# Optimization experiments

Hardware: AMD Instinct MI355X
Metric: run time of the kernel (lower is better)

Reference implementation:

```python
import jax, jax.numpy as jnp
import numpy as np

B, KL, XL, DIM, H, PB = 4, 128, 4096, 256, 8, 8
HD = DIM // H
SCALE = HD ** -0.5
N_DIS = 64 + 2


def setup_inputs() -> dict:
    key = jax.random.key(0)
    ks = jax.random.split(key, 10)
    x = jax.random.normal(ks[0], (B, XL, DIM), jnp.float32)
    kernal = jax.random.normal(ks[1], (B, KL, DIM), jnp.float32)
    rd = jax.random.randint(ks[2], (B, KL, XL), 0, N_DIS)
    polar_pos = jax.random.randint(ks[3], (B, KL, XL), 0, PB)
    att_mask = jax.random.uniform(ks[4], (B, H, XL, KL)) < 0.1
    W_qkv = jax.random.normal(ks[5], (DIM, 3 * DIM), jnp.float32) * 0.02
    dis_embed = jax.random.normal(ks[6], (N_DIS, H), jnp.float32) * 0.02
    polar_emb = jax.random.normal(ks[7], (PB, 1), jnp.float32) * 0.02
    W_proj = jax.random.normal(ks[8], (DIM, DIM), jnp.float32) * 0.02
    b_proj = jnp.zeros((DIM,), jnp.float32)
    return dict(x=x, kernal=kernal, rd=rd, polar_pos=polar_pos, att_mask=att_mask,
                W_qkv=W_qkv, dis_embed=dis_embed, polar_emb=polar_emb,
                W_proj=W_proj, b_proj=b_proj)


def _heads(t, h):
    b, n, d = t.shape
    return t.reshape(b, n, h, d // h).transpose(0, 2, 1, 3)  # b h n hd


def reference(x, kernal, rd, polar_pos, att_mask, W_qkv, dis_embed, polar_emb, W_proj, b_proj):
    b, xl, dim = x.shape
    kl = kernal.shape[1]
    h = H
    scale = (dim // h) ** -0.5

    q, k, v = [_heads(t, h) for t in jnp.split(x @ W_qkv, 3, axis=-1)]        # b h xl hd
    k_q, k_k, k_v = [_heads(t, h) for t in jnp.split(kernal @ W_qkv, 3, axis=-1)]  # b h kl hd

    rd_e = dis_embed[rd].transpose(0, 3, 1, 2)  # (b,kl,xl,h) -> (b,h,kl,xl)

    # kernel -> x attention scores
    k_x_attn = jnp.einsum('bhkd,bhxd->bhkx', k_q, k) * scale  # b h kl xl

    # main orientation: one-hot-weighted |attn| reduced over x, argmax over polar bins
    pp = jnp.broadcast_to(polar_pos[:, None], (b, h, kl, xl))  # b h kl xl
    polar_hot = jax.nn.one_hot(pp, PB, dtype=k_x_attn.dtype)   # b h kl xl o
    ori_sum = jnp.einsum('bhkx,bhkxo->bhko', jnp.abs(k_x_attn), polar_hot)
    main_ori = jnp.argmax(ori_sum, axis=-1)                    # b h kl
    new_polar = pp - main_ori[..., None]
    new_polar = jnp.where(new_polar < 0, new_polar + PB, new_polar)
    polar_bias = polar_emb[new_polar, 0]                       # b h kl xl

    mask_k = att_mask.transpose(0, 1, 3, 2)                    # b h kl xl
    k_x_attn = jnp.where(mask_k, jnp.asarray(-1e6, k_x_attn.dtype), k_x_attn)
    attn_k = jax.nn.softmax(k_x_attn + rd_e + polar_bias, axis=-1)
    k_out = jnp.einsum('bhkx,bhxd->bhkd', attn_k, v)
    k_out = k_out.transpose(0, 2, 1, 3).reshape(b, kl, dim) @ W_proj + b_proj

    # x -> kernel attention scores
    x_k_attn = jnp.einsum('bhxd,bhkd->bhxk', q, k_k) * scale   # b h xl kl
    x_k_attn = jnp.where(att_mask, jnp.asarray(-1e9, x_k_attn.dtype), x_k_attn)
    x_k_attn = jax.nn.softmax(x_k_attn + rd_e.transpose(0, 1, 3, 2)
                              + polar_bias.transpose(0, 1, 3, 2), axis=-1)
    x_out = jnp.einsum('bhxk,bhkd->bhxd', x_k_attn, k_v)
    x_out = x_out.transpose(0, 2, 1, 3).reshape(b, xl, dim) @ W_proj + b_proj

    return (x_out, k_out)
```

## Files before the change

kernel.cpp:

```cpp
#include <hip/hip_runtime.h>
#include <hip/hip_bf16.h>

#define B_    4
#define KL_   128
#define XL_   4096
#define DIM_  256
#define H_    8
#define HD_   32
#define PB_   8
#define NDIS_ 66
#define TDIM_ 768
#define SCALE_ 0.17677669529663687f
#define NS_   4
#define XCH_  (XL_ / NS_)
#define NCH2_ 64
#define KC2_  16

typedef float v4f __attribute__((ext_vector_type(4)));
typedef short v8s __attribute__((ext_vector_type(8)));

__device__ __forceinline__ unsigned short f2bf(float f) {
    __hip_bfloat16 h = __float2bfloat16(f);
    return __builtin_bit_cast(unsigned short, h);
}
__device__ __forceinline__ float bf2f(unsigned short u) {
    return __bfloat162float(__builtin_bit_cast(__hip_bfloat16, u));
}
__device__ __forceinline__ void cvt_hilo(float v, unsigned short& hi, unsigned short& lo) {
    hi = f2bf(v);
    lo = f2bf(v - bf2f(hi));
}

__global__ __launch_bounds__(256) void pack_mask(const int* __restrict__ att_mask,
                                                 unsigned int* __restrict__ mbits) {
    size_t wid = (size_t)blockIdx.x * 256 + threadIdx.x;
    const int* src = &att_mask[wid * 32];
    unsigned bits = 0;
#pragma unroll
    for (int i = 0; i < 8; ++i) {
        int4 m4 = *(const int4*)&src[i * 4];
        bits |= (m4.x ? 1u : 0u) << (i * 4 + 0);
        bits |= (m4.y ? 1u : 0u) << (i * 4 + 1);
        bits |= (m4.z ? 1u : 0u) << (i * 4 + 2);
        bits |= (m4.w ? 1u : 0u) << (i * 4 + 3);
    }
    mbits[wid] = bits;
}

__global__ __launch_bounds__(256) void cvt_mat(const float* __restrict__ A,
                                               unsigned short* __restrict__ Ah,
                                               unsigned short* __restrict__ Al,
                                               size_t n4) {
    size_t i = ((size_t)blockIdx.x * 256 + threadIdx.x);
    if (i >= n4) return;
    float4 v = *(const float4*)&A[i * 4];
    ushort4 h, l;
    cvt_hilo(v.x, h.x, l.x);
    cvt_hilo(v.y, h.y, l.y);
    cvt_hilo(v.z, h.z, l.z);
    cvt_hilo(v.w, h.w, l.w);
    *(ushort4*)&Ah[i * 4] = h;
    *(ushort4*)&Al[i * 4] = l;
}

__global__ __launch_bounds__(256) void cvt_wT(const float* __restrict__ W,
                                              unsigned short* __restrict__ Wh,
                                              unsigned short* __restrict__ Wl,
                                              int K, int N) {
    int n = blockIdx.x, k = threadIdx.x;
    float v = W[(size_t)k * N + n];
    unsigned short h, l;
    cvt_hilo(v, h, l);
    Wh[(size_t)n * K + k] = h;
    Wl[(size_t)n * K + k] = l;
}

__global__ __launch_bounds__(256) void cvt_kq(const float* __restrict__ qkv_k,
                                              unsigned short* __restrict__ Kqh_g,
                                              unsigned short* __restrict__ Kql_g) {
    const int bh = blockIdx.x;
    const int b = bh >> 3, h = bh & 7;
    const int tid = threadIdx.x;
    const int k = tid >> 1, dg = (tid & 1) * 16;
    const float* src = &qkv_k[((size_t)(b * KL_ + k)) * TDIM_ + h * HD_ + dg];
    unsigned short hi[16], lo[16];
#pragma unroll
    for (int j4 = 0; j4 < 4; ++j4) {
        float4 v = *(const float4*)&src[j4 * 4];
        cvt_hilo(v.x, hi[j4 * 4 + 0], lo[j4 * 4 + 0]);
        cvt_hilo(v.y, hi[j4 * 4 + 1], lo[j4 * 4 + 1]);
        cvt_hilo(v.z, hi[j4 * 4 + 2], lo[j4 * 4 + 2]);
        cvt_hilo(v.w, hi[j4 * 4 + 3], lo[j4 * 4 + 3]);
    }
    unsigned short* dh = &Kqh_g[((size_t)bh * KL_ + k) * HD_ + dg];
    unsigned short* dl = &Kql_g[((size_t)bh * KL_ + k) * HD_ + dg];
    *(uint4*)&dh[0] = *(uint4*)&hi[0];
    *(uint4*)&dh[8] = *(uint4*)&hi[8];
    *(uint4*)&dl[0] = *(uint4*)&lo[0];
    *(uint4*)&dl[8] = *(uint4*)&lo[8];
}

__global__ __launch_bounds__(256) void gemm_mfma(const unsigned short* __restrict__ Ah,
                                                 const unsigned short* __restrict__ Al,
                                                 const unsigned short* __restrict__ Bh,
                                                 const unsigned short* __restrict__ Bl,
                                                 float* __restrict__ C,
                                                 const float* __restrict__ bias,
                                                 int M, int N, int K) {
    __shared__ __align__(16) unsigned short Ah_s[128 * 32];
    __shared__ __align__(16) unsigned short Al_s[128 * 32];
    __shared__ __align__(16) unsigned short Bh_s[128 * 32];
    __shared__ __align__(16) unsigned short Bl_s[128 * 32];
    const int tid = threadIdx.x;
    const int w = tid >> 6, lane = tid & 63;
    const int c = lane & 15, q = lane >> 4;
    const int bm = blockIdx.y * 128, bn = blockIdx.x * 128;

    const int lrow = lane >> 2;
    const int lcol = (lane & 3) * 8;

    v4f acc[2][8] = {};
    for (int k0 = 0; k0 < K; k0 += 32) {
        __syncthreads();
#pragma unroll
        for (int i = 0; i < 2; ++i) {
            const int chunk = w * 2 + i;
            const int row = chunk * 16 + lrow;
            const size_t ga = (size_t)(bm + row) * K + k0 + lcol;
            const size_t gb = (size_t)(bn + row) * K + k0 + lcol;
            const int lo = chunk * 512;
            __builtin_amdgcn_global_load_lds(
                (const __attribute__((address_space(1))) unsigned int*)&Ah[ga],
                (__attribute__((address_space(3))) unsigned int*)&Ah_s[lo], 16, 0, 0);
            __builtin_amdgcn_global_load_lds(
                (const __attribute__((address_space(1))) unsigned int*)&Al[ga],
                (__attribute__((address_space(3))) unsigned int*)&Al_s[lo], 16, 0, 0);
            __builtin_amdgcn_global_load_lds(
                (const __attribute__((address_space(1))) unsigned int*)&Bh[gb],
                (__attribute__((address_space(3))) unsigned int*)&Bh_s[lo], 16, 0, 0);
            __builtin_amdgcn_global_load_lds(
                (const __attribute__((address_space(1))) unsigned int*)&Bl[gb],
                (__attribute__((address_space(3))) unsigned int*)&Bl_s[lo], 16, 0, 0);
        }
        asm volatile("s_waitcnt vmcnt(0)" ::: "memory");
        __syncthreads();
        v8s afh[2], afl[2];
#pragma unroll
        for (int mt = 0; mt < 2; ++mt) {
            afh[mt] = *(v8s*)&Ah_s[(w * 32 + mt * 16 + c) * 32 + q * 8];
            afl[mt] = *(v8s*)&Al_s[(w * 32 + mt * 16 + c) * 32 + q * 8];
        }
#pragma unroll
        for (int nt = 0; nt < 8; ++nt) {
            v8s bfh = *(v8s*)&Bh_s[(nt * 16 + c) * 32 + q * 8];
            v8s bfl = *(v8s*)&Bl_s[(nt * 16 + c) * 32 + q * 8];
#pragma unroll
            for (int mt = 0; mt < 2; ++mt) {
                acc[mt][nt] = __builtin_amdgcn_mfma_f32_16x16x32_bf16(afl[mt], bfh, acc[mt][nt], 0, 0, 0);
                acc[mt][nt] = __builtin_amdgcn_mfma_f32_16x16x32_bf16(afh[mt], bfl, acc[mt][nt], 0, 0, 0);
                acc[mt][nt] = __builtin_amdgcn_mfma_f32_16x16x32_bf16(afh[mt], bfh, acc[mt][nt], 0, 0, 0);
            }
        }
    }
#pragma unroll
    for (int mt = 0; mt < 2; ++mt) {
#pragma unroll
        for (int nt = 0; nt < 8; ++nt) {
            int col = bn + nt * 16 + c;
            float bv = bias ? bias[col] : 0.0f;
#pragma unroll
            for (int r = 0; r < 4; ++r) {
                int row = bm + w * 32 + mt * 16 + q * 4 + r;
                C[(size_t)row * N + col] = acc[mt][nt][r] + bv;
            }
        }
    }
}

__global__ __launch_bounds__(256) void gemm64(const float* __restrict__ A,
                                              const float* __restrict__ Bw,
                                              float* __restrict__ C,
                                              const float* __restrict__ bias,
                                              int M, int N, int K) {
    __shared__ __align__(16) float As[16][68];
    __shared__ __align__(16) float Bs[16][64];
    const int tid = threadIdx.x;
    const int tx = tid & 15, ty = tid >> 4;
    const int bn = blockIdx.x * 64, bm = blockIdx.y * 64;
    const int am = tid >> 2, ac = tid & 3;
    float acc[4][4] = {};
    for (int k0 = 0; k0 < K; k0 += 16) {
        float4 a4 = *(const float4*)&A[(size_t)(bm + am) * K + k0 + ac * 4];
        As[ac * 4 + 0][am] = a4.x;
        As[ac * 4 + 1][am] = a4.y;
        As[ac * 4 + 2][am] = a4.z;
        As[ac * 4 + 3][am] = a4.w;
        *(float4*)&Bs[ty][tx * 4] = *(const float4*)&Bw[(size_t)(k0 + ty) * N + bn + tx * 4];
        __syncthreads();
#pragma unroll
        for (int kk = 0; kk < 16; ++kk) {
            float4 av = *(const float4*)&As[kk][ty * 4];
            float4 bv = *(const float4*)&Bs[kk][tx * 4];
            float a[4] = {av.x, av.y, av.z, av.w};
            float b[4] = {bv.x, bv.y, bv.z, bv.w};
#pragma unroll
            for (int i = 0; i < 4; ++i)
#pragma unroll
                for (int j = 0; j < 4; ++j) acc[i][j] += a[i] * b[j];
        }
        __syncthreads();
    }
#pragma unroll
    for (int i = 0; i < 4; ++i) {
        int m = bm + ty * 4 + i;
#pragma unroll
        for (int j = 0; j < 4; ++j) {
            int n = bn + tx * 4 + j;
            float v = acc[i][j];
            if (bias) v += bias[n];
            C[(size_t)m * N + n] = v;
        }
    }
}

__global__ __launch_bounds__(256) void score_bins_mfma4(const float* __restrict__ qkv_x,
                                                        const unsigned short* __restrict__ Kqh_g,
                                                        const unsigned short* __restrict__ Kql_g,
                                                        const int* __restrict__ rd,
                                                        const int* __restrict__ polar_pos,
                                                        const unsigned int* __restrict__ mbits,
                                                        const float* __restrict__ dis_embed,
                                                        __hip_bfloat16* __restrict__ Sg,
                                                        float* __restrict__ binspart) {
    const int b = blockIdx.z, h = blockIdx.y, xc = blockIdx.x;
    const int x0 = xc * 64;
    const int tid = threadIdx.x;
    const int w = tid >> 6, lane = tid & 63;
    const int c15 = lane & 15, q = lane >> 4;
    const size_t bh = (size_t)(b * H_ + h);

    __shared__ unsigned int mskb[64][5];
    __shared__ float de_h[NDIS_];
    __shared__ float binsL[8][4][16][PB_];

    {
        int xr = tid >> 2, kg = tid & 3;
        mskb[xr][kg] = mbits[(bh * XL_ + x0 + xr) * 4 + kg];
    }
    if (tid < NDIS_) de_h[tid] = dis_embed[tid * H_ + h];
    __syncthreads();

    v8s axh, axl;
    {
        const float* src = &qkv_x[((size_t)b * XL_ + x0 + w * 16 + c15) * TDIM_ + DIM_ + h * HD_ + q * 8];
        float4 v0 = *(const float4*)&src[0];
        float4 v1 = *(const float4*)&src[4];
        float vv[8] = {v0.x, v0.y, v0.z, v0.w, v1.x, v1.y, v1.z, v1.w};
#pragma unroll
        for (int j = 0; j < 8; ++j) {
            unsigned short hi, lo;
            cvt_hilo(vv[j], hi, lo);
            ((short*)&axh)[j] = (short)hi;
            ((short*)&axl)[j] = (short)lo;
        }
    }

    v8s bqh[2], bql[2];
    int4 r4[2], p4[2];
    auto load_nt = [&](int nt, int s) {
        const int k = nt * 16 + c15;
        const size_t kqoff = (bh * KL_ + k) * HD_ + q * 8;
        bqh[s] = *(const v8s*)&Kqh_g[kqoff];
        bql[s] = *(const v8s*)&Kql_g[kqoff];
        const size_t rowoff = ((size_t)(b * KL_ + k)) * XL_ + x0 + w * 16 + q * 4;
        r4[s] = *(const int4*)&rd[rowoff];
        p4[s] = *(const int4*)&polar_pos[rowoff];
    };
    load_nt(0, 0);

#pragma unroll
    for (int nt = 0; nt < 8; ++nt) {
        const int s = nt & 1;
        if (nt < 7) load_nt(nt + 1, s ^ 1);

        const int k = nt * 16 + c15;
        v4f D = {0.f, 0.f, 0.f, 0.f};
        D = __builtin_amdgcn_mfma_f32_16x16x32_bf16(axl, bqh[s], D, 0, 0, 0);
        D = __builtin_amdgcn_mfma_f32_16x16x32_bf16(axh, bql[s], D, 0, 0, 0);
        D = __builtin_amdgcn_mfma_f32_16x16x32_bf16(axh, bqh[s], D, 0, 0, 0);

        float bins[PB_] = {};
        {
            int rv[4] = {r4[s].x, r4[s].y, r4[s].z, r4[s].w};
            int pv[4] = {p4[s].x, p4[s].y, p4[s].z, p4[s].w};
            ushort4 pack;
#pragma unroll
            for (int r = 0; r < 4; ++r) {
                float sc = D[r] * SCALE_;
                float a = fabsf(sc);
                int pp = pv[r];
#pragma unroll
                for (int pb = 0; pb < PB_; ++pb) bins[pb] += (pp == pb) ? a : 0.0f;
                int xloc = w * 16 + q * 4 + r;
                int mbit = (mskb[xloc][k >> 5] >> (k & 31)) & 1;
                float sp = (mbit ? -1e6f : sc) + de_h[rv[r]];
                ((unsigned short*)&pack)[r] = f2bf(sp);
            }
            *(ushort4*)((unsigned short*)Sg + (bh * KL_ + k) * XL_ + x0 + w * 16 + q * 4) = pack;
        }

#pragma unroll
        for (int pb = 0; pb < PB_; ++pb) {
            bins[pb] += __shfl_xor(bins[pb], 16);
            bins[pb] += __shfl_xor(bins[pb], 32);
        }
        if (q == 0) {
#pragma unroll
            for (int pb = 0; pb < PB_; ++pb) binsL[nt][w][c15][pb] = bins[pb];
        }
    }
    __syncthreads();
    {
        int k = tid >> 1, half = tid & 1;
        int nt = k >> 4, c = k & 15;
        float4 s = {0.f, 0.f, 0.f, 0.f};
#pragma unroll
        for (int w4 = 0; w4 < 4; ++w4) {
            float4 v = *(float4*)&binsL[nt][w4][c][half * 4];
            s.x += v.x; s.y += v.y; s.z += v.z; s.w += v.w;
        }
        *(float4*)&binspart[(bh * KL_ + k) * (NCH2_ * PB_) + xc * PB_ + half * 4] = s;
    }
}

__global__ __launch_bounds__(256) void bins_argmax(const float* __restrict__ binspart,
                                                   int* __restrict__ main_ori) {
    const int w = threadIdx.x >> 6, lane = threadIdx.x & 63;
    const int row = blockIdx.x * 4 + w;
    float s[PB_];
#pragma unroll
    for (int pb = 0; pb < PB_; ++pb) s[pb] = 0.0f;
    if (lane < NCH2_) {
        const float* bp = &binspart[(size_t)row * (NCH2_ * PB_) + lane * PB_];
#pragma unroll
        for (int pb = 0; pb < PB_; ++pb) s[pb] = bp[pb];
    }
#pragma unroll
    for (int m = 1; m < 64; m <<= 1)
#pragma unroll
        for (int pb = 0; pb < PB_; ++pb) s[pb] += __shfl_xor(s[pb], m);
    if (lane == 0) {
        float best = s[0];
        int bi = 0;
#pragma unroll
        for (int pb = 1; pb < PB_; ++pb)
            if (s[pb] > best) { best = s[pb]; bi = pb; }
        main_ori[row] = bi;
    }
}

__global__ __launch_bounds__(256) void flash_cached2(const float* __restrict__ qkv_x,
                                                     const __hip_bfloat16* __restrict__ Sg,
                                                     const int* __restrict__ polar_pos,
                                                     const float* __restrict__ polar_emb,
                                                     const int* __restrict__ main_ori,
                                                     float* __restrict__ part) {
    const int b = blockIdx.z, h = blockIdx.y;
    const int kch = blockIdx.x / NS_, xc = blockIdx.x % NS_;
    const int k0 = kch * KC2_;
    const int tid = threadIdx.x;
    const int ki = tid >> 4, xt = tid & 15;

    __shared__ __align__(16) float4 vs[64][9];
    __shared__ int pol_s[KC2_][68];
    __shared__ float pe[PB_];

    if (tid < PB_) pe[tid] = polar_emb[tid];
    const size_t xbase = (size_t)b * XL_;
    const size_t bh = (size_t)(b * H_ + h);
    const size_t row_k = bh * KL_ + k0 + ki;
    const int mo = main_ori[row_k];
    const int xbeg = xc * XCH_;

    float l = 0.f;
    float4 acc[8] = {};
    __syncthreads();
    for (int t = 0; t < XCH_ / 64; ++t) {
        const int x0 = xbeg + t * 64;
        __syncthreads();
#pragma unroll
        for (int i = 0; i < 2; ++i) {
            int id = tid + 256 * i;
            int row = id >> 3, c = id & 7;
            vs[row][c] = *(const float4*)&qkv_x[(xbase + x0 + row) * TDIM_ + 2 * DIM_ + h * HD_ + c * 4];
        }
        {
            int kk = tid >> 4, c = tid & 15;
            *(int4*)&pol_s[kk][c * 4] =
                *(const int4*)&polar_pos[(size_t)(b * KL_ + k0 + kk) * XL_ + x0 + c * 4];
        }
        __syncthreads();
#pragma unroll
        for (int j = 0; j < 4; ++j) {
            int xl = xt + 16 * j;
            int x = x0 + xl;
            float sp = __bfloat162float(Sg[row_k * XL_ + x]);
            int pp = pol_s[ki][xl];
            int np = pp - mo;
            np += (np >> 31) & PB_;
            float p = __expf(sp + pe[np]);
            l += p;
#pragma unroll
            for (int c = 0; c < 8; ++c) {
                float4 v = vs[xl][c];
                acc[c].x += p * v.x; acc[c].y += p * v.y;
                acc[c].z += p * v.z; acc[c].w += p * v.w;
            }
        }
    }
#pragma unroll
    for (int m = 1; m < 16; m <<= 1) {
        l += __shfl_xor(l, m, 16);
#pragma unroll
        for (int c = 0; c < 8; ++c) {
            acc[c].x += __shfl_xor(acc[c].x, m, 16);
            acc[c].y += __shfl_xor(acc[c].y, m, 16);
            acc[c].z += __shfl_xor(acc[c].z, m, 16);
            acc[c].w += __shfl_xor(acc[c].w, m, 16);
        }
    }
    if (xt == 0) {
        float* dst = &part[(size_t)(row_k * NS_ + xc) * 36];
#pragma unroll
        for (int c = 0; c < 8; ++c) *(float4*)&dst[c * 4] = acc[c];
        dst[32] = l;
    }
}

__global__ __launch_bounds__(256) void merge_cached(const float* __restrict__ part,
                                                    float* __restrict__ kout_pre) {
    const int tid = threadIdx.x;
    const int ri = tid >> 5, d = tid & 31;
    const int row = blockIdx.x * 8 + ri;
    float l = 0.f, a = 0.f;
#pragma unroll
    for (int c = 0; c < NS_; ++c) {
        const float* p = &part[(size_t)(row * NS_ + c) * 36];
        l += p[32];
        a += p[d];
    }
    int k = row & (KL_ - 1);
    int bh = row >> 7;
    int h = bh & (H_ - 1), b = bh >> 3;
    kout_pre[(size_t)(b * KL_ + k) * DIM_ + h * HD_ + d] = a / l;
}

__global__ __launch_bounds__(256) void attn_x_mfma(const float* __restrict__ qkv_x,
                                                   const float* __restrict__ qkv_k,
                                                   const int* __restrict__ rd,
                                                   const int* __restrict__ polar_pos,
                                                   const unsigned int* __restrict__ mbits,
                                                   const float* __restrict__ dis_embed,
                                                   const float* __restrict__ polar_emb,
                                                   const int* __restrict__ main_ori,
                                                   unsigned short* __restrict__ oh,
                                                   unsigned short* __restrict__ ol) {
    const int b = blockIdx.z, h = blockIdx.y;
    const int x0 = blockIdx.x * 64;
    const int tid = threadIdx.x;
    const int wave = tid >> 6, lane = tid & 63;
    const int c = lane & 15, q = lane >> 4;

    __shared__ __align__(16) unsigned short Kk_s[KL_][40];
    __shared__ __align__(16) unsigned short VT_s[HD_][136];
    __shared__ __align__(16) unsigned short P_s[4][16][136];
    __shared__ unsigned short rp_s[KL_][72];
    __shared__ unsigned int msk_s[64][5];
    __shared__ float de_h[NDIS_];
    __shared__ float pe[PB_];
    __shared__ int mo_s[KL_];

    const size_t bh = (size_t)(b * H_ + h);
    if (tid < NDIS_) de_h[tid] = dis_embed[tid * H_ + h];
    if (tid < PB_) pe[tid] = polar_emb[tid];
    if (tid < KL_) mo_s[tid] = main_ori[bh * KL_ + tid];

    {
        int row = tid >> 1, half = tid & 1;
        const float* src = &qkv_k[(size_t)(b * KL_ + row) * TDIM_ + h * HD_ + half * 16];
#pragma unroll
        for (int j = 0; j < 16; ++j) Kk_s[row][half * 16 + j] = f2bf(src[DIM_ + j]);
#pragma unroll
        for (int j = 0; j < 16; ++j) VT_s[half * 16 + j][row] = f2bf(src[2 * DIM_ + j]);
    }
    {
        int xr = tid >> 2, kg = tid & 3;
        msk_s[xr][kg] = mbits[(bh * XL_ + x0 + xr) * 4 + kg];
    }
    __syncthreads();

#pragma unroll
    for (int i = 0; i < 8; ++i) {
        int id = tid + 256 * i;
        int k = id >> 4, cc = id & 15;
        size_t gb = (size_t)(b * KL_ + k) * XL_ + x0 + cc * 4;
        int4 r4 = *(const int4*)&rd[gb];
        int4 p4 = *(const int4*)&polar_pos[gb];
        int mo = mo_s[k];
        int n0 = p4.x - mo; n0 += (n0 >> 31) & PB_;
        int n1 = p4.y - mo; n1 += (n1 >> 31) & PB_;
        int n2 = p4.z - mo; n2 += (n2 >> 31) & PB_;
        int n3 = p4.w - mo; n3 += (n3 >> 31) & PB_;
        rp_s[k][cc * 4 + 0] = (unsigned short)(r4.x | (n0 << 8));
        rp_s[k][cc * 4 + 1] = (unsigned short)(r4.y | (n1 << 8));
        rp_s[k][cc * 4 + 2] = (unsigned short)(r4.z | (n2 << 8));
        rp_s[k][cc * 4 + 3] = (unsigned short)(r4.w | (n3 << 8));
    }
    __syncthreads();

    v8s aq;
    {
        const float* qp = &qkv_x[(size_t)(b * XL_ + x0 + wave * 16 + c) * TDIM_ + h * HD_ + q * 8];
        float4 q0 = *(const float4*)&qp[0];
        float4 q1 = *(const float4*)&qp[4];
        aq[0] = (short)f2bf(q0.x); aq[1] = (short)f2bf(q0.y);
        aq[2] = (short)f2bf(q0.z); aq[3] = (short)f2bf(q0.w);
        aq[4] = (short)f2bf(q1.x); aq[5] = (short)f2bf(q1.y);
        aq[6] = (short)f2bf(q1.z); aq[7] = (short)f2bf(q1.w);
    }

    v4f S[8];
#pragma unroll
    for (int t = 0; t < 8; ++t) {
        v8s bk = *(v8s*)&Kk_s[t * 16 + c][q * 8];
        S[t] = __builtin_amdgcn_mfma_f32_16x16x32_bf16(aq, bk, (v4f){0.f, 0.f, 0.f, 0.f}, 0, 0, 0);
    }

    const int xloc = wave * 16;
    float lr[4] = {0.f, 0.f, 0.f, 0.f};
#pragma unroll
    for (int t = 0; t < 8; ++t) {
#pragma unroll
        for (int r = 0; r < 4; ++r) {
            int krow = t * 16 + c;
            int xrow = q * 4 + r;
            unsigned short rp = rp_s[krow][xloc + xrow];
            int mbit = (msk_s[xloc + xrow][krow >> 5] >> (krow & 31)) & 1;
            float sval = S[t][r] * SCALE_;
            float tval = (mbit ? -25.0f : sval) + de_h[rp & 0x7f] + pe[(rp >> 8) & 7];
            float p = __expf(tval);
            unsigned short pb = f2bf(p);
            P_s[wave][xrow][krow] = pb;
            lr[r] += bf2f(pb);
        }
    }
#pragma unroll
    for (int r = 0; r < 4; ++r) {
#pragma unroll
        for (int m = 1; m < 16; m <<= 1) lr[r] += __shfl_xor(lr[r], m);
    }
    __syncthreads();

    v4f O0 = {0.f, 0.f, 0.f, 0.f}, O1 = {0.f, 0.f, 0.f, 0.f};
#pragma unroll
    for (int kc = 0; kc < 4; ++kc) {
        v8s ap = *(v8s*)&P_s[wave][c][kc * 32 + q * 8];
        v8s bv0 = *(v8s*)&VT_s[c][kc * 32 + q * 8];
        v8s bv1 = *(v8s*)&VT_s[16 + c][kc * 32 + q * 8];
        O0 = __builtin_amdgcn_mfma_f32_16x16x32_bf16(ap, bv0, O0, 0, 0, 0);
        O1 = __builtin_amdgcn_mfma_f32_16x16x32_bf16(ap, bv1, O1, 0, 0, 0);
    }

#pragma unroll
    for (int r = 0; r < 4; ++r) {
        int xg = x0 + wave * 16 + q * 4 + r;
        float inv = 1.0f / lr[r];
        size_t obase = (size_t)(b * XL_ + xg) * DIM_ + h * HD_;
        float v0 = O0[r] * inv;
        float v1 = O1[r] * inv;
        unsigned short h0, l0, h1, l1;
        cvt_hilo(v0, h0, l0);
        cvt_hilo(v1, h1, l1);
        oh[obase + c] = h0;
        ol[obase + c] = l0;
        oh[obase + 16 + c] = h1;
        ol[obase + 16 + c] = l1;
    }
}

extern "C" void kernel_launch(void* const* d_in, const int* in_sizes, int n_in,
                              void* d_out, int out_size, void* d_ws, size_t ws_size,
                              hipStream_t stream) {
    const float* x         = (const float*)d_in[0];
    const float* kernal    = (const float*)d_in[1];
    const int* rd          = (const int*)d_in[2];
    const int* polar_pos   = (const int*)d_in[3];
    const int* att_mask    = (const int*)d_in[4];
    const float* W_qkv     = (const float*)d_in[5];
    const float* dis_embed = (const float*)d_in[6];
    const float* polar_emb = (const float*)d_in[7];
    const float* W_proj    = (const float*)d_in[8];
    const float* b_proj    = (const float*)d_in[9];
    float* out             = (float*)d_out;

    char* base = (char*)d_ws;
    size_t off = 0;
    auto alloc = [&](size_t bytes) { void* p = base + off; off = (off + bytes + 255) & ~255ULL; return p; };
    float* qkv_x    = (float*)alloc((size_t)B_ * XL_ * TDIM_ * 4);
    float* qkv_k    = (float*)alloc((size_t)B_ * KL_ * TDIM_ * 4);
    float* xout_pre = (float*)alloc((size_t)B_ * XL_ * DIM_ * 4);
    float* kout_pre = (float*)alloc((size_t)B_ * KL_ * DIM_ * 4);
    int* main_ori   = (int*)alloc(B_ * H_ * KL_ * 4);
    float* part     = (float*)alloc((size_t)B_ * H_ * KL_ * NS_ * 36 * 4);
    __hip_bfloat16* Sg = (__hip_bfloat16*)alloc((size_t)B_ * H_ * KL_ * XL_ * 2);
    unsigned short* wph = (unsigned short*)alloc((size_t)DIM_ * DIM_ * 2);
    unsigned short* wpl = (unsigned short*)alloc((size_t)DIM_ * DIM_ * 2);
    unsigned int* mbits = (unsigned int*)alloc((size_t)B_ * H_ * XL_ * (KL_ / 32) * 4);

    float* binspart = xout_pre;
    const size_t MX = (size_t)B_ * XL_;
    unsigned short* xh = (unsigned short*)Sg;
    unsigned short* xl_ = xh + MX * DIM_;
    unsigned short* wqh = (unsigned short*)part;
    unsigned short* wql = wqh + (size_t)TDIM_ * DIM_;
    unsigned short* kqh_g = wqh + 2 * (size_t)TDIM_ * DIM_;
    unsigned short* kql_g = kqh_g + (size_t)B_ * H_ * KL_ * HD_;
    unsigned short* oh = (unsigned short*)Sg;
    unsigned short* ol = oh + MX * DIM_;

    pack_mask<<<dim3((B_ * H_ * XL_ * (KL_ / 32)) / 256), 256, 0, stream>>>(att_mask, mbits);
    cvt_mat<<<dim3((MX * DIM_ / 4 + 255) / 256), 256, 0, stream>>>(x, xh, xl_, MX * DIM_ / 4);
    cvt_wT<<<dim3(TDIM_), DIM_, 0, stream>>>(W_qkv, wqh, wql, DIM_, TDIM_);
    cvt_wT<<<dim3(DIM_), DIM_, 0, stream>>>(W_proj, wph, wpl, DIM_, DIM_);

    gemm_mfma<<<dim3(TDIM_ / 128, MX / 128), 256, 0, stream>>>(
        xh, xl_, wqh, wql, qkv_x, nullptr, MX, TDIM_, DIM_);
    gemm64<<<dim3(TDIM_ / 64, (B_ * KL_) / 64), 256, 0, stream>>>(
        kernal, W_qkv, qkv_k, nullptr, B_ * KL_, TDIM_, DIM_);
    cvt_kq<<<dim3(B_ * H_), 256, 0, stream>>>(qkv_k, kqh_g, kql_g);

    score_bins_mfma4<<<dim3(NCH2_, H_, B_), 256, 0, stream>>>(
        qkv_x, kqh_g, kql_g, rd, polar_pos, mbits, dis_embed, Sg, binspart);
    bins_argmax<<<dim3(B_ * H_ * KL_ / 4), 256, 0, stream>>>(binspart, main_ori);
    flash_cached2<<<dim3((KL_ / KC2_) * NS_, H_, B_), 256, 0, stream>>>(
        qkv_x, Sg, polar_pos, polar_emb, main_ori, part);
    merge_cached<<<dim3(B_ * H_ * KL_ / 8), 256, 0, stream>>>(part, kout_pre);

    attn_x_mfma<<<dim3(XL_ / 64, H_, B_), 256, 0, stream>>>(
        qkv_x, qkv_k, rd, polar_pos, mbits, dis_embed, polar_emb, main_ori, oh, ol);

    gemm_mfma<<<dim3(DIM_ / 128, MX / 128), 256, 0, stream>>>(
        oh, ol, wph, wpl, out, b_proj, MX, DIM_, DIM_);
    gemm64<<<dim3(DIM_ / 64, (B_ * KL_) / 64), 256, 0, stream>>>(
        kout_pre, W_proj, out + (size_t)B_ * XL_ * DIM_, b_proj, B_ * KL_, DIM_, DIM_);
}
```

Baseline: 352.7 us.

## Precompute bf16 K and V^T once; stage score tile writes through LDS

Adds bf16 K and transposed V buffers built once in cvt_kq, so attn_x_mfma reads MFMA operands straight from global memory. This removes the per-block fp32 load, convert and LDS transpose that every one of the 2048 blocks repeated. In score_bins_mfma4, each score tile is staged in shared memory before being written to Sg as contiguous row segments instead of scattered 8-byte strided stores. The cost is an extra __syncthreads per tile iteration and global operand loads in place of LDS reads inside attn_x.

```diff
diff --git a/kernel.cpp b/kernel.cpp
--- a/kernel.cpp
+++ b/kernel.cpp
@@ -77,7 +77,9 @@
 
 __global__ __launch_bounds__(256) void cvt_kq(const float* __restrict__ qkv_k,
                                               unsigned short* __restrict__ Kqh_g,
-                                              unsigned short* __restrict__ Kql_g) {
+                                              unsigned short* __restrict__ Kql_g,
+                                              unsigned short* __restrict__ Kk_bf,
+                                              unsigned short* __restrict__ VT_bf) {
     const int bh = blockIdx.x;
     const int b = bh >> 3, h = bh & 7;
     const int tid = threadIdx.x;
@@ -98,6 +100,21 @@
     *(uint4*)&dh[8] = *(uint4*)&hi[8];
     *(uint4*)&dl[0] = *(uint4*)&lo[0];
     *(uint4*)&dl[8] = *(uint4*)&lo[8];
+    unsigned short kk[16];
+#pragma unroll
+    for (int j4 = 0; j4 < 4; ++j4) {
+        float4 v = *(const float4*)&src[DIM_ + j4 * 4];
+        kk[j4 * 4 + 0] = f2bf(v.x);
+        kk[j4 * 4 + 1] = f2bf(v.y);
+        kk[j4 * 4 + 2] = f2bf(v.z);
+        kk[j4 * 4 + 3] = f2bf(v.w);
+    }
+    unsigned short* dk = &Kk_bf[((size_t)bh * KL_ + k) * HD_ + dg];
+    *(uint4*)&dk[0] = *(uint4*)&kk[0];
+    *(uint4*)&dk[8] = *(uint4*)&kk[8];
+#pragma unroll
+    for (int j = 0; j < 16; ++j)
+        VT_bf[((size_t)bh * HD_ + dg + j) * KL_ + k] = f2bf(src[2 * DIM_ + j]);
 }
 
 __global__ __launch_bounds__(256) void gemm_mfma(const unsigned short* __restrict__ Ah,
@@ -242,6 +259,7 @@
     __shared__ unsigned int mskb[64][5];
     __shared__ float de_h[NDIS_];
     __shared__ float binsL[8][4][16][PB_];
+    __shared__ __align__(16) unsigned short Ss[2][16][72];
 
     {
         int xr = tid >> 2, kg = tid & 3;
@@ -306,7 +324,7 @@
                 float sp = (mbit ? -1e6f : sc) + de_h[rv[r]];
                 ((unsigned short*)&pack)[r] = f2bf(sp);
             }
-            *(ushort4*)((unsigned short*)Sg + (bh * KL_ + k) * XL_ + x0 + w * 16 + q * 4) = pack;
+            *(ushort4*)&Ss[s][c15][w * 16 + q * 4] = pack;
         }
 
 #pragma unroll
@@ -317,6 +335,14 @@
         if (q == 0) {
 #pragma unroll
             for (int pb = 0; pb < PB_; ++pb) binsL[nt][w][c15][pb] = bins[pb];
+        }
+
+        __syncthreads();
+        {
+            int row = tid >> 4, seg = tid & 15;
+            unsigned short* dst = (unsigned short*)Sg +
+                (bh * KL_ + nt * 16 + row) * XL_ + x0 + seg * 4;
+            *(uint2*)dst = *(const uint2*)&Ss[s][row][seg * 4];
         }
     }
     __syncthreads();
@@ -456,7 +482,8 @@
 }
 
 __global__ __launch_bounds__(256) void attn_x_mfma(const float* __restrict__ qkv_x,
-                                                   const float* __restrict__ qkv_k,
+                                                   const unsigned short* __restrict__ Kk_bf,
+                                                   const unsigned short* __restrict__ VT_bf,
                                                    const int* __restrict__ rd,
                                                    const int* __restrict__ polar_pos,
                                                    const unsigned int* __restrict__ mbits,
@@ -471,8 +498,6 @@
     const int wave = tid >> 6, lane = tid & 63;
     const int c = lane & 15, q = lane >> 4;
 
-    __shared__ __align__(16) unsigned short Kk_s[KL_][40];
-    __shared__ __align__(16) unsigned short VT_s[HD_][136];
     __shared__ __align__(16) unsigned short P_s[4][16][136];
     __shared__ unsigned short rp_s[KL_][72];
     __shared__ unsigned int msk_s[64][5];
@@ -484,15 +509,6 @@
     if (tid < NDIS_) de_h[tid] = dis_embed[tid * H_ + h];
     if (tid < PB_) pe[tid] = polar_emb[tid];
     if (tid < KL_) mo_s[tid] = main_ori[bh * KL_ + tid];
-
-    {
-        int row = tid >> 1, half = tid & 1;
-        const float* src = &qkv_k[(size_t)(b * KL_ + row) * TDIM_ + h * HD_ + half * 16];
-#pragma unroll
-        for (int j = 0; j < 16; ++j) Kk_s[row][half * 16 + j] = f2bf(src[DIM_ + j]);
-#pragma unroll
-        for (int j = 0; j < 16; ++j) VT_s[half * 16 + j][row] = f2bf(src[2 * DIM_ + j]);
-    }
     {
         int xr = tid >> 2, kg = tid & 3;
         msk_s[xr][kg] = mbits[(bh * XL_ + x0 + xr) * 4 + kg];
@@ -529,10 +545,11 @@
         aq[6] = (short)f2bf(q1.z); aq[7] = (short)f2bf(q1.w);
     }
 
+    const unsigned short* KkB = &Kk_bf[(size_t)bh * KL_ * HD_];
     v4f S[8];
 #pragma unroll
     for (int t = 0; t < 8; ++t) {
-        v8s bk = *(v8s*)&Kk_s[t * 16 + c][q * 8];
+        v8s bk = *(const v8s*)&KkB[(size_t)(t * 16 + c) * HD_ + q * 8];
         S[t] = __builtin_amdgcn_mfma_f32_16x16x32_bf16(aq, bk, (v4f){0.f, 0.f, 0.f, 0.f}, 0, 0, 0);
     }
 
@@ -561,12 +578,13 @@
     }
     __syncthreads();
 
+    const unsigned short* VTB = &VT_bf[(size_t)bh * HD_ * KL_];
     v4f O0 = {0.f, 0.f, 0.f, 0.f}, O1 = {0.f, 0.f, 0.f, 0.f};
 #pragma unroll
     for (int kc = 0; kc < 4; ++kc) {
         v8s ap = *(v8s*)&P_s[wave][c][kc * 32 + q * 8];
-        v8s bv0 = *(v8s*)&VT_s[c][kc * 32 + q * 8];
-        v8s bv1 = *(v8s*)&VT_s[16 + c][kc * 32 + q * 8];
+        v8s bv0 = *(const v8s*)&VTB[(size_t)c * KL_ + kc * 32 + q * 8];
+        v8s bv1 = *(const v8s*)&VTB[(size_t)(16 + c) * KL_ + kc * 32 + q * 8];
         O0 = __builtin_amdgcn_mfma_f32_16x16x32_bf16(ap, bv0, O0, 0, 0, 0);
         O1 = __builtin_amdgcn_mfma_f32_16x16x32_bf16(ap, bv1, O1, 0, 0, 0);
     }
@@ -616,6 +634,8 @@
     unsigned short* wph = (unsigned short*)alloc((size_t)DIM_ * DIM_ * 2);
     unsigned short* wpl = (unsigned short*)alloc((size_t)DIM_ * DIM_ * 2);
     unsigned int* mbits = (unsigned int*)alloc((size_t)B_ * H_ * XL_ * (KL_ / 32) * 4);
+    unsigned short* Kk_bf = (unsigned short*)alloc((size_t)B_ * H_ * KL_ * HD_ * 2);
+    unsigned short* VT_bf = (unsigned short*)alloc((size_t)B_ * H_ * HD_ * KL_ * 2);
 
     float* binspart = xout_pre;
     const size_t MX = (size_t)B_ * XL_;
@@ -637,7 +657,7 @@
         xh, xl_, wqh, wql, qkv_x, nullptr, MX, TDIM_, DIM_);
     gemm64<<<dim3(TDIM_ / 64, (B_ * KL_) / 64), 256, 0, stream>>>(
         kernal, W_qkv, qkv_k, nullptr, B_ * KL_, TDIM_, DIM_);
-    cvt_kq<<<dim3(B_ * H_), 256, 0, stream>>>(qkv_k, kqh_g, kql_g);
+    cvt_kq<<<dim3(B_ * H_), 256, 0, stream>>>(qkv_k, kqh_g, kql_g, Kk_bf, VT_bf);
 
     score_bins_mfma4<<<dim3(NCH2_, H_, B_), 256, 0, stream>>>(
         qkv_x, kqh_g, kql_g, rd, polar_pos, mbits, dis_embed, Sg, binspart);
@@ -647,7 +667,7 @@
     merge_cached<<<dim3(B_ * H_ * KL_ / 8), 256, 0, stream>>>(part, kout_pre);
 
     attn_x_mfma<<<dim3(XL_ / 64, H_, B_), 256, 0, stream>>>(
-        qkv_x, qkv_k, rd, polar_pos, mbits, dis_embed, polar_emb, main_ori, oh, ol);
+        qkv_x, Kk_bf, VT_bf, rd, polar_pos, mbits, dis_embed, polar_emb, main_ori, oh, ol);
 
     gemm_mfma<<<dim3(DIM_ / 128, MX / 128), 256, 0, stream>>>(
         oh, ol, wph, wpl, out, b_proj, MX, DIM_, DIM_);
```

Measured after the change: 345.9 us. Within noise of the previous version (-1.9%).
